# Kernel tuning notes

Hardware: AMD Instinct MI355X
Metric: run time of the kernel (lower is better)

Reference implementation:

```python
import jax, jax.numpy as jnp
import numpy as np

HEAD_NUM = 16

def setup_inputs() -> dict:
    key = jax.random.key(0)
    ks = jax.random.split(key, 5)
    B, N, D = 2, 2048, 1024
    x = jax.random.normal(ks[0], (B, N, D), dtype=jnp.float32)
    scale = 0.02
    W_q = jax.random.normal(ks[1], (D, D), dtype=jnp.float32) * scale
    W_k = jax.random.normal(ks[2], (D, D), dtype=jnp.float32) * scale
    W_v = jax.random.normal(ks[3], (D, D), dtype=jnp.float32) * scale
    W_o = jax.random.normal(ks[4], (D, D), dtype=jnp.float32) * scale
    return {"x": x, "W_q": W_q, "W_k": W_k, "W_v": W_v, "W_o": W_o}

def reference(x, W_q, W_k, W_v, W_o):
    B, N, D = x.shape
    H = HEAD_NUM
    hd = D // H  # head_dim
    inv_sqrt_hd = 1.0 / np.sqrt(hd).astype(np.float32)

    def split_head(t):
        # einops 'b n (d h) -> b h n d' : head index is the INNER factor
        return t.reshape(B, N, hd, H).transpose(0, 3, 1, 2)  # [B,H,N,hd]

    # nn.Linear(bias=False): y = x @ W.T
    Q = split_head(x @ W_q.T)
    K = split_head(x @ W_k.T)
    V = split_head(x @ W_v.T)

    scores = jnp.einsum('bhnd,bhmd->bhnm', Q, K) * inv_sqrt_hd  # [B,H,N,N]
    attn = jax.nn.softmax(scores, axis=-1)
    heads = jnp.einsum('bhnm,bhmd->bhnd', attn, V)  # [B,H,N,hd]

    # einops 'b h n d -> b n (h d)' : head index is the OUTER factor here
    concat = heads.transpose(0, 2, 1, 3).reshape(B, N, D)
    return concat @ W_o.T
```

## Files before the change

### kernel.cpp

```cpp
#include <hip/hip_runtime.h>
#include <hip/hip_bf16.h>

typedef __bf16 bf16_t;
typedef __attribute__((ext_vector_type(8))) __bf16 bf16x8;
typedef __attribute__((ext_vector_type(4))) __bf16 bf16x4;
typedef __attribute__((ext_vector_type(4))) float f32x4;
typedef __attribute__((ext_vector_type(16))) float f32x16;

#define MFMA16(A,B,C) __builtin_amdgcn_mfma_f32_16x16x32_bf16((A),(B),(C),0,0,0)
#define MFMA32(A,B,C) __builtin_amdgcn_mfma_f32_32x32x16_bf16((A),(B),(C),0,0,0)

#define BATCH 2
#define SEQ 2048
#define DMODEL 1024
#define NHEAD 16
#define HDIM 64
#define MROWS (BATCH * SEQ)

__device__ __forceinline__ void async16(const bf16_t* g, bf16_t* l) {
    __builtin_amdgcn_global_load_lds(
        (const __attribute__((address_space(1))) unsigned int*)g,
        (__attribute__((address_space(3))) unsigned int*)l, 16, 0, 0);
}

__device__ __forceinline__ bf16x8 ldsA32(const bf16_t* base, int row, int chunk) {
    return *(const bf16x8*)&base[row * 32 + ((chunk ^ ((row >> 1) & 3)) << 3)];
}

__device__ __forceinline__ unsigned pk(float a, float b) {
    union { unsigned u; bf16_t h[2]; } t;
    t.h[0] = (bf16_t)a;
    t.h[1] = (bf16_t)b;
    return t.u;
}

__global__ void split_kernel(const float* __restrict__ x, const float* __restrict__ Wq,
                             const float* __restrict__ Wk, const float* __restrict__ Wv,
                             const float* __restrict__ Wo, bf16_t* __restrict__ xh,
                             bf16_t* __restrict__ wh) {
    int blk = blockIdx.x;
    if (blk < 4096) {
        int i = blk * 256 + threadIdx.x;
        f32x4 v = ((const f32x4*)x)[i];
        bf16x4 h;
#pragma unroll
        for (int c = 0; c < 4; ++c) h[c] = (bf16_t)v[c];
        ((bf16x4*)xh)[i] = h;
        return;
    }
    int e = blk - 4096;
    int z = e >> 10;
    int i = (e & 1023) * 256 + threadIdx.x;
    const float* src = (z == 0) ? Wq : (z == 1) ? Wk : (z == 2) ? Wv : Wo;
    const float scale = (z == 0) ? 0.125f * 1.44269504088896f : 1.0f;
    int row = i >> 8, col4 = i & 255;
    int r_src;
    if (z < 3) {
        int h = row >> 6, d = row & 63;
        r_src = 16 * d + h;
    } else {
        r_src = row;
    }
    f32x4 v = ((const f32x4*)src)[r_src * 256 + col4];
    bf16x4 h4;
#pragma unroll
    for (int c = 0; c < 4; ++c) h4[c] = (bf16_t)(v[c] * scale);
    ((bf16x4*)(wh + (size_t)z * DMODEL * DMODEL))[i] = h4;
}

__global__ __launch_bounds__(256)
void gemm_qkv_kernel(const bf16_t* __restrict__ Ah, const bf16_t* __restrict__ Bh0,
                     bf16_t* __restrict__ Coh0, bf16_t* __restrict__ Vt,
                     int M, int Nn, int Kk) {
    __shared__ __align__(16) bf16_t smem[2][8192];

    const int id = blockIdx.x;
    const int xcd = id & 7;
    const int t = id >> 3;
    const int n0i = t & 7;
    const int u = t >> 3;
    const int z = u >> 2;
    const int m0g = u & 3;
    const int m0 = (m0g * 8 + xcd) * 128;
    const int n0 = n0i * 128;

    const bf16_t* Bh = Bh0 + (size_t)z * Nn * Kk;
    const int tid = threadIdx.x;
    const int wave = tid >> 6, lane = tid & 63, lq = lane >> 4, ln = lane & 15;
    const int wr = wave >> 1, wc = wave & 1;

    const bf16_t* g_ptr[4];
    int l_off[4];
#pragma unroll
    for (int q = 0; q < 4; ++q) {
        int e = wave * 4 + q;
        int a = e >> 3, uu = e & 7;
        int C = uu * 64 + lane;
        int r = C >> 2, p = C & 3;
        int c = p ^ ((r >> 1) & 3);
        g_ptr[q] = (a == 0 ? Ah + (size_t)(m0 + r) * Kk
                           : Bh + (size_t)(n0 + r) * Kk) + c * 8;
        l_off[q] = a * 4096 + uu * 512;
    }

    f32x4 acc[4][4] = {};

#pragma unroll
    for (int q = 0; q < 4; ++q)
        async16(g_ptr[q], &smem[0][l_off[q]]);

    const int NIT = Kk / 32;
    for (int j = 0; j < NIT; ++j) {
        __syncthreads();
        if (j + 1 < NIT) {
#pragma unroll
            for (int q = 0; q < 4; ++q)
                async16(g_ptr[q] + (j + 1) * 32, &smem[(j + 1) & 1][l_off[q]]);
        }
        const bf16_t* cur = smem[j & 1];

        bf16x8 ah[4], bh[4];
#pragma unroll
        for (int tt = 0; tt < 4; ++tt) {
            ah[tt] = ldsA32(cur, wr * 64 + tt * 16 + ln, lq);
            bh[tt] = ldsA32(cur + 4096, wc * 64 + tt * 16 + ln, lq);
        }
#pragma unroll
        for (int tm = 0; tm < 4; ++tm)
#pragma unroll
            for (int tn = 0; tn < 4; ++tn)
                acc[tm][tn] = MFMA16(ah[tm], bh[tn], acc[tm][tn]);
    }

    if (z != 2) {
#pragma unroll
        for (int tm = 0; tm < 4; ++tm)
#pragma unroll
            for (int tn = 0; tn < 4; ++tn)
#pragma unroll
                for (int p = 0; p < 4; ++p) {
                    int gm = m0 + wr * 64 + tm * 16 + lq * 4 + p;
                    int gn = n0 + wc * 64 + tn * 16 + ln;
                    Coh0[(size_t)z * M * Nn + (size_t)gm * Nn + gn] =
                        (bf16_t)acc[tm][tn][p];
                }
    } else {
#pragma unroll
        for (int tm = 0; tm < 4; ++tm)
#pragma unroll
            for (int tn = 0; tn < 4; ++tn) {
                int gn = n0 + wc * 64 + tn * 16 + ln;
                int hh = gn >> 6, dd = gn & 63;
                int gm0 = m0 + wr * 64 + tm * 16 + lq * 4;
                int bb = gm0 >> 11, nn = gm0 & 2047;
                bf16x4 v4;
#pragma unroll
                for (int p = 0; p < 4; ++p) v4[p] = (bf16_t)acc[tm][tn][p];
                *(bf16x4*)&Vt[(((size_t)(bb * NHEAD + hh)) * HDIM + dd) * SEQ + nn] = v4;
            }
    }
}

__global__ __launch_bounds__(256)
void gemm_out_kernel(const bf16_t* __restrict__ Ah, const bf16_t* __restrict__ Bh,
                     float* __restrict__ Cf, int M, int Nn, int Kk) {
    __shared__ __align__(16) bf16_t smem[2][6144];

    const int id = blockIdx.x;
    const int xcd = id & 7;
    const int t = id >> 3;
    const int n0i = t & 7;
    const int m0g = t >> 3;
    const int m0 = (m0g * 8 + xcd) * 64;
    const int n0 = n0i * 128;

    const int tid = threadIdx.x;
    const int wave = tid >> 6, lane = tid & 63, lq = lane >> 4, ln = lane & 15;
    const int wr = wave >> 1, wc = wave & 1;

    const bf16_t* g_ptr[3];
    int l_off[3];
#pragma unroll
    for (int q = 0; q < 3; ++q) {
        int e = wave * 3 + q;
        const bf16_t* arr;
        int u, rowbase, lb;
        if (e < 4) { arr = Ah; u = e;     rowbase = m0; lb = 0; }
        else       { arr = Bh; u = e - 4; rowbase = n0; lb = 2048; }
        int r = u * 16 + (lane >> 2), p = lane & 3;
        int c = p ^ ((r >> 1) & 3);
        g_ptr[q] = arr + (size_t)(rowbase + r) * Kk + c * 8;
        l_off[q] = lb + u * 512;
    }

    f32x4 acc[2][4] = {};

#pragma unroll
    for (int q = 0; q < 3; ++q)
        async16(g_ptr[q], &smem[0][l_off[q]]);

    const int NIT = Kk / 32;
    for (int j = 0; j < NIT; ++j) {
        __syncthreads();
        if (j + 1 < NIT) {
#pragma unroll
            for (int q = 0; q < 3; ++q)
                async16(g_ptr[q] + (j + 1) * 32, &smem[(j + 1) & 1][l_off[q]]);
        }
        const bf16_t* cur = smem[j & 1];

        bf16x8 ah[2], bh[4];
#pragma unroll
        for (int tt = 0; tt < 2; ++tt)
            ah[tt] = ldsA32(cur, wr * 32 + tt * 16 + ln, lq);
#pragma unroll
        for (int tt = 0; tt < 4; ++tt)
            bh[tt] = ldsA32(cur + 2048, wc * 64 + tt * 16 + ln, lq);
#pragma unroll
        for (int tm = 0; tm < 2; ++tm)
#pragma unroll
            for (int tn = 0; tn < 4; ++tn)
                acc[tm][tn] = MFMA16(ah[tm], bh[tn], acc[tm][tn]);
    }

#pragma unroll
    for (int tm = 0; tm < 2; ++tm)
#pragma unroll
        for (int tn = 0; tn < 4; ++tn)
#pragma unroll
            for (int p = 0; p < 4; ++p) {
                int gm = m0 + wr * 32 + tm * 16 + lq * 4 + p;
                int gn = n0 + wc * 64 + tn * 16 + ln;
                Cf[(size_t)gm * Nn + gn] = acc[tm][tn][p];
            }
}

__global__ __launch_bounds__(512, 4)
void attn_kernel(const bf16_t* __restrict__ Qh, const bf16_t* __restrict__ Kh,
                 const bf16_t* __restrict__ Vt, bf16_t* __restrict__ Ch) {
    __shared__ __align__(16) bf16_t smem[2][2][8192];

    const int id = blockIdx.x;
    const int bh = ((id >> 7) << 3) | (id & 7);
    const int qt = (id >> 3) & 15;
    const int b = bh >> 4, h = bh & 15;
    const int q0 = qt * 128;
    const int tid = threadIdx.x;
    const int g = tid >> 8;
    const int wv = (tid >> 6) & 3;
    const int lane = tid & 63;
    const int ln32 = lane & 31, hl = lane >> 5;

    bf16x8 qfh[4];
    {
        size_t qrow = ((size_t)(b * SEQ + q0 + wv * 32 + ln32)) * DMODEL +
                      h * HDIM + hl * 8;
#pragma unroll
        for (int c = 0; c < 4; ++c)
            qfh[c] = *(const bf16x8*)&Qh[qrow + c * 16];
    }

    const int xrow = ln32 * 64;
    int xc[4];
#pragma unroll
    for (int c = 0; c < 4; ++c)
        xc[c] = (((2 * c + hl) ^ (ln32 & 7)) << 3) + xrow;

    bf16_t* gsm = &smem[g][0][0];
    const bf16_t* g_cur[4];
    int l_off[4];
    size_t g_step[4];
#pragma unroll
    for (int q = 0; q < 4; ++q) {
        int e = wv * 4 + q;
        int a = e >> 3, u = e & 7;
        int r = u * 8 + (lane >> 3), p = lane & 7;
        int c = p ^ (r & 7);
        if (a == 0) {
            g_cur[q] = Kh + ((size_t)(b * SEQ + g * 1024 + r)) * DMODEL +
                       h * HDIM + c * 8;
            l_off[q] = u * 512;
            g_step[q] = (size_t)64 * DMODEL;
        } else {
            g_cur[q] = Vt + ((size_t)(bh * HDIM + r)) * SEQ + g * 1024 + c * 8;
            l_off[q] = 4096 + u * 512;
            g_step[q] = 64;
        }
    }

    f32x16 o[2];
#pragma unroll
    for (int dt = 0; dt < 2; ++dt)
#pragma unroll
        for (int r = 0; r < 16; ++r) o[dt][r] = 0.0f;
    float rs = 0.0f;

#pragma unroll
    for (int q = 0; q < 4; ++q) {
        async16(g_cur[q], gsm + l_off[q]);
        g_cur[q] += g_step[q];
    }

    for (int j = 0; j < 16; ++j) {
        __syncthreads();
        if (j < 15) {
#pragma unroll
            for (int q = 0; q < 4; ++q) {
                async16(g_cur[q], gsm + ((j + 1) & 1) * 8192 + l_off[q]);
                g_cur[q] += g_step[q];
            }
        }
        const bf16_t* Kc = gsm + (j & 1) * 8192;
        const bf16_t* Vc = Kc + 4096;

        bf16x8 pfrag[4];
#pragma unroll
        for (int kt = 0; kt < 2; ++kt) {
            f32x16 st;
#pragma unroll
            for (int r = 0; r < 16; ++r) st[r] = 0.0f;
#pragma unroll
            for (int c = 0; c < 4; ++c) {
                bf16x8 kh = *(const bf16x8*)&Kc[kt * 2048 + xc[c]];
                st = MFMA32(kh, qfh[c], st);
            }
            float pexp[16];
#pragma unroll
            for (int r = 0; r < 16; ++r) {
                pexp[r] = __builtin_amdgcn_exp2f(st[r]);
                rs += pexp[r];
            }
#pragma unroll
            for (int s1 = 0; s1 < 2; ++s1) {
                unsigned lo01 = pk(pexp[8 * s1 + 0], pexp[8 * s1 + 1]);
                unsigned lo23 = pk(pexp[8 * s1 + 2], pexp[8 * s1 + 3]);
                unsigned hi01 = pk(pexp[8 * s1 + 4], pexp[8 * s1 + 5]);
                unsigned hi23 = pk(pexp[8 * s1 + 6], pexp[8 * s1 + 7]);
                unsigned sa = hl ? lo01 : hi01;
                unsigned sb = hl ? lo23 : hi23;
                unsigned ra = (unsigned)__shfl_xor((int)sa, 32);
                unsigned rb = (unsigned)__shfl_xor((int)sb, 32);
                union { bf16x8 v; unsigned u[4]; } outv;
                outv.u[0] = hl ? ra : lo01;
                outv.u[1] = hl ? rb : lo23;
                outv.u[2] = hl ? hi01 : ra;
                outv.u[3] = hl ? hi23 : rb;
                pfrag[kt * 2 + s1] = outv.v;
            }
        }
#pragma unroll
        for (int s = 0; s < 4; ++s) {
            bf16x8 va0 = *(const bf16x8*)&Vc[xc[s]];
            bf16x8 va1 = *(const bf16x8*)&Vc[2048 + xc[s]];
            o[0] = MFMA32(va0, pfrag[s], o[0]);
            o[1] = MFMA32(va1, pfrag[s], o[1]);
        }
    }

    rs += __shfl_xor(rs, 32);

    __syncthreads();
    float* cbuf = (float*)smem;
    float* rbuf = cbuf + 8192;
    if (g == 1) {
#pragma unroll
        for (int dt = 0; dt < 2; ++dt)
#pragma unroll
            for (int r = 0; r < 16; ++r) {
                int d = dt * 32 + (r & 3) + 8 * (r >> 2) + 4 * hl;
                cbuf[d * 128 + wv * 32 + ln32] = o[dt][r];
            }
        if (hl == 0) rbuf[wv * 32 + ln32] = rs;
    }
    __syncthreads();
    float inv = 0.0f;
    if (g == 0) {
#pragma unroll
        for (int dt = 0; dt < 2; ++dt)
#pragma unroll
            for (int r = 0; r < 16; ++r) {
                int d = dt * 32 + (r & 3) + 8 * (r >> 2) + 4 * hl;
                o[dt][r] += cbuf[d * 128 + wv * 32 + ln32];
            }
        inv = 1.0f / (rs + rbuf[wv * 32 + ln32]);
    }
    __syncthreads();
    float* fbuf = (float*)smem;
    if (g == 0) {
#pragma unroll
        for (int dh = 0; dh < 2; ++dh)
#pragma unroll
            for (int r = 0; r < 16; ++r) {
                int d_loc = (r & 3) + 8 * (r >> 2) + 4 * hl;
                fbuf[dh * 4224 + wv * 1056 + ln32 * 33 + d_loc] = o[dh][r] * inv;
            }
    }
    __syncthreads();
    {
        int gw = tid >> 6;
        int dh = gw >> 2, w = gw & 3;
#pragma unroll
        for (int qq = 0; qq < 16; ++qq) {
            int qrow = hl * 16 + qq;
            float v = fbuf[dh * 4224 + w * 1056 + qrow * 33 + ln32];
            size_t gidx = ((size_t)(b * SEQ + q0 + w * 32 + qrow)) * DMODEL +
                          h * HDIM + dh * 32 + ln32;
            Ch[gidx] = (bf16_t)v;
        }
    }
}

extern "C" void kernel_launch(void* const* d_in, const int* in_sizes, int n_in,
                              void* d_out, int out_size, void* d_ws, size_t ws_size,
                              hipStream_t stream) {
    const float* x  = (const float*)d_in[0];
    const float* Wq = (const float*)d_in[1];
    const float* Wk = (const float*)d_in[2];
    const float* Wv = (const float*)d_in[3];
    const float* Wo = (const float*)d_in[4];
    float* out = (float*)d_out;

    char* ws = (char*)d_ws;
    size_t off = 0;
    auto alloc = [&](size_t bytes) -> bf16_t* {
        bf16_t* p = (bf16_t*)(ws + off);
        off += (bytes + 255) & ~(size_t)255;
        return p;
    };
    const size_t XE = (size_t)MROWS * DMODEL;
    const size_t WE = (size_t)DMODEL * DMODEL;

    bf16_t* xh  = alloc(XE * 2);
    bf16_t* wh  = alloc(4 * WE * 2);
    bf16_t* qnh = alloc(3 * XE * 2);
    bf16_t* vth = alloc(XE * 2);
    bf16_t* ch  = alloc(XE * 2);
    (void)ws_size; (void)in_sizes; (void)n_in; (void)out_size;

    split_kernel<<<8192, 256, 0, stream>>>(x, Wq, Wk, Wv, Wo, xh, wh);

    gemm_qkv_kernel<<<768, 256, 0, stream>>>(xh, wh, qnh, vth, MROWS, DMODEL, DMODEL);

    attn_kernel<<<512, 512, 0, stream>>>(qnh, qnh + XE, vth, ch);

    gemm_out_kernel<<<512, 256, 0, stream>>>(ch, wh + 3 * WE, out, MROWS, DMODEL, DMODEL);
}
```

Baseline: 179.4 us.

## Halve attention block threads, each wave computing two 32-row query tiles

The attention kernel now runs 256 threads (4 waves) per block instead of 512. Each wave handles two 32-query sub-tiles, so every K and V fragment read from LDS is reused across two MFMAs, and each wave issues twice as many async K/V loads. The aim is to cut LDS read traffic per MFMA and the per-wave overhead. In exchange, register pressure roughly doubles for accumulators and Q fragments, and there are fewer waves available to hide latency.

```diff
diff --git a/kernel.cpp b/kernel.cpp
--- a/kernel.cpp
+++ b/kernel.cpp
@@ -235,7 +235,7 @@
             }
 }
 
-__global__ __launch_bounds__(512, 4)
+__global__ __launch_bounds__(256, 2)
 void attn_kernel(const bf16_t* __restrict__ Qh, const bf16_t* __restrict__ Kh,
                  const bf16_t* __restrict__ Vt, bf16_t* __restrict__ Ch) {
     __shared__ __align__(16) bf16_t smem[2][2][8192];
@@ -246,18 +246,20 @@
     const int b = bh >> 4, h = bh & 15;
     const int q0 = qt * 128;
     const int tid = threadIdx.x;
-    const int g = tid >> 8;
-    const int wv = (tid >> 6) & 3;
+    const int wave = tid >> 6;
+    const int g = wave >> 1;
+    const int wg = wave & 1;
     const int lane = tid & 63;
     const int ln32 = lane & 31, hl = lane >> 5;
 
-    bf16x8 qfh[4];
-    {
-        size_t qrow = ((size_t)(b * SEQ + q0 + wv * 32 + ln32)) * DMODEL +
+    bf16x8 qfh[2][4];
+#pragma unroll
+    for (int s = 0; s < 2; ++s) {
+        size_t qrow = ((size_t)(b * SEQ + q0 + wg * 64 + s * 32 + ln32)) * DMODEL +
                       h * HDIM + hl * 8;
 #pragma unroll
         for (int c = 0; c < 4; ++c)
-            qfh[c] = *(const bf16x8*)&Qh[qrow + c * 16];
+            qfh[s][c] = *(const bf16x8*)&Qh[qrow + c * 16];
     }
 
     const int xrow = ln32 * 64;
@@ -267,12 +269,12 @@
         xc[c] = (((2 * c + hl) ^ (ln32 & 7)) << 3) + xrow;
 
     bf16_t* gsm = &smem[g][0][0];
-    const bf16_t* g_cur[4];
-    int l_off[4];
-    size_t g_step[4];
-#pragma unroll
-    for (int q = 0; q < 4; ++q) {
-        int e = wv * 4 + q;
+    const bf16_t* g_cur[8];
+    int l_off[8];
+    size_t g_step[8];
+#pragma unroll
+    for (int q = 0; q < 8; ++q) {
+        int e = wg * 8 + q;
         int a = e >> 3, u = e & 7;
         int r = u * 8 + (lane >> 3), p = lane & 7;
         int c = p ^ (r & 7);
@@ -288,15 +290,17 @@
         }
     }
 
-    f32x16 o[2];
-#pragma unroll
-    for (int dt = 0; dt < 2; ++dt)
-#pragma unroll
-        for (int r = 0; r < 16; ++r) o[dt][r] = 0.0f;
-    float rs = 0.0f;
-
-#pragma unroll
-    for (int q = 0; q < 4; ++q) {
+    f32x16 o[2][2];
+#pragma unroll
+    for (int s = 0; s < 2; ++s)
+#pragma unroll
+        for (int dt = 0; dt < 2; ++dt)
+#pragma unroll
+            for (int r = 0; r < 16; ++r) o[s][dt][r] = 0.0f;
+    float rs[2] = {0.0f, 0.0f};
+
+#pragma unroll
+    for (int q = 0; q < 8; ++q) {
         async16(g_cur[q], gsm + l_off[q]);
         g_cur[q] += g_step[q];
     }
@@ -305,7 +309,7 @@
         __syncthreads();
         if (j < 15) {
 #pragma unroll
-            for (int q = 0; q < 4; ++q) {
+            for (int q = 0; q < 8; ++q) {
                 async16(g_cur[q], gsm + ((j + 1) & 1) * 8192 + l_off[q]);
                 g_cur[q] += g_step[q];
             }
@@ -313,100 +317,121 @@
         const bf16_t* Kc = gsm + (j & 1) * 8192;
         const bf16_t* Vc = Kc + 4096;
 
-        bf16x8 pfrag[4];
+        bf16x8 pfrag[2][4];
 #pragma unroll
         for (int kt = 0; kt < 2; ++kt) {
-            f32x16 st;
-#pragma unroll
-            for (int r = 0; r < 16; ++r) st[r] = 0.0f;
+            f32x16 st0, st1;
+#pragma unroll
+            for (int r = 0; r < 16; ++r) { st0[r] = 0.0f; st1[r] = 0.0f; }
 #pragma unroll
             for (int c = 0; c < 4; ++c) {
                 bf16x8 kh = *(const bf16x8*)&Kc[kt * 2048 + xc[c]];
-                st = MFMA32(kh, qfh[c], st);
-            }
-            float pexp[16];
-#pragma unroll
-            for (int r = 0; r < 16; ++r) {
-                pexp[r] = __builtin_amdgcn_exp2f(st[r]);
-                rs += pexp[r];
-            }
-#pragma unroll
-            for (int s1 = 0; s1 < 2; ++s1) {
-                unsigned lo01 = pk(pexp[8 * s1 + 0], pexp[8 * s1 + 1]);
-                unsigned lo23 = pk(pexp[8 * s1 + 2], pexp[8 * s1 + 3]);
-                unsigned hi01 = pk(pexp[8 * s1 + 4], pexp[8 * s1 + 5]);
-                unsigned hi23 = pk(pexp[8 * s1 + 6], pexp[8 * s1 + 7]);
-                unsigned sa = hl ? lo01 : hi01;
-                unsigned sb = hl ? lo23 : hi23;
-                unsigned ra = (unsigned)__shfl_xor((int)sa, 32);
-                unsigned rb = (unsigned)__shfl_xor((int)sb, 32);
-                union { bf16x8 v; unsigned u[4]; } outv;
-                outv.u[0] = hl ? ra : lo01;
-                outv.u[1] = hl ? rb : lo23;
-                outv.u[2] = hl ? hi01 : ra;
-                outv.u[3] = hl ? hi23 : rb;
-                pfrag[kt * 2 + s1] = outv.v;
-            }
-        }
-#pragma unroll
-        for (int s = 0; s < 4; ++s) {
-            bf16x8 va0 = *(const bf16x8*)&Vc[xc[s]];
-            bf16x8 va1 = *(const bf16x8*)&Vc[2048 + xc[s]];
-            o[0] = MFMA32(va0, pfrag[s], o[0]);
-            o[1] = MFMA32(va1, pfrag[s], o[1]);
-        }
-    }
-
-    rs += __shfl_xor(rs, 32);
+                st0 = MFMA32(kh, qfh[0][c], st0);
+                st1 = MFMA32(kh, qfh[1][c], st1);
+            }
+#pragma unroll
+            for (int s = 0; s < 2; ++s) {
+                float pexp[16];
+#pragma unroll
+                for (int r = 0; r < 16; ++r) {
+                    pexp[r] = __builtin_amdgcn_exp2f(s == 0 ? st0[r] : st1[r]);
+                    rs[s] += pexp[r];
+                }
+#pragma unroll
+                for (int s1 = 0; s1 < 2; ++s1) {
+                    unsigned lo01 = pk(pexp[8 * s1 + 0], pexp[8 * s1 + 1]);
+                    unsigned lo23 = pk(pexp[8 * s1 + 2], pexp[8 * s1 + 3]);
+                    unsigned hi01 = pk(pexp[8 * s1 + 4], pexp[8 * s1 + 5]);
+                    unsigned hi23 = pk(pexp[8 * s1 + 6], pexp[8 * s1 + 7]);
+                    unsigned sa = hl ? lo01 : hi01;
+                    unsigned sb = hl ? lo23 : hi23;
+                    unsigned ra = (unsigned)__shfl_xor((int)sa, 32);
+                    unsigned rb = (unsigned)__shfl_xor((int)sb, 32);
+                    union { bf16x8 v; unsigned u[4]; } outv;
+                    outv.u[0] = hl ? ra : lo01;
+                    outv.u[1] = hl ? rb : lo23;
+                    outv.u[2] = hl ? hi01 : ra;
+                    outv.u[3] = hl ? hi23 : rb;
+                    pfrag[s][kt * 2 + s1] = outv.v;
+                }
+            }
+        }
+#pragma unroll
+        for (int sg = 0; sg < 4; ++sg) {
+            bf16x8 va0 = *(const bf16x8*)&Vc[xc[sg]];
+            bf16x8 va1 = *(const bf16x8*)&Vc[2048 + xc[sg]];
+            o[0][0] = MFMA32(va0, pfrag[0][sg], o[0][0]);
+            o[1][0] = MFMA32(va0, pfrag[1][sg], o[1][0]);
+            o[0][1] = MFMA32(va1, pfrag[0][sg], o[0][1]);
+            o[1][1] = MFMA32(va1, pfrag[1][sg], o[1][1]);
+        }
+    }
+
+    rs[0] += __shfl_xor(rs[0], 32);
+    rs[1] += __shfl_xor(rs[1], 32);
 
     __syncthreads();
     float* cbuf = (float*)smem;
     float* rbuf = cbuf + 8192;
     if (g == 1) {
 #pragma unroll
-        for (int dt = 0; dt < 2; ++dt)
-#pragma unroll
-            for (int r = 0; r < 16; ++r) {
-                int d = dt * 32 + (r & 3) + 8 * (r >> 2) + 4 * hl;
-                cbuf[d * 128 + wv * 32 + ln32] = o[dt][r];
-            }
-        if (hl == 0) rbuf[wv * 32 + ln32] = rs;
+        for (int s = 0; s < 2; ++s) {
+            int qcol = wg * 64 + s * 32 + ln32;
+#pragma unroll
+            for (int dt = 0; dt < 2; ++dt)
+#pragma unroll
+                for (int r = 0; r < 16; ++r) {
+                    int d = dt * 32 + (r & 3) + 8 * (r >> 2) + 4 * hl;
+                    cbuf[d * 128 + qcol] = o[s][dt][r];
+                }
+            if (hl == 0) rbuf[qcol] = rs[s];
+        }
     }
     __syncthreads();
-    float inv = 0.0f;
+    float inv[2] = {0.0f, 0.0f};
     if (g == 0) {
 #pragma unroll
-        for (int dt = 0; dt < 2; ++dt)
-#pragma unroll
-            for (int r = 0; r < 16; ++r) {
-                int d = dt * 32 + (r & 3) + 8 * (r >> 2) + 4 * hl;
-                o[dt][r] += cbuf[d * 128 + wv * 32 + ln32];
-            }
-        inv = 1.0f / (rs + rbuf[wv * 32 + ln32]);
+        for (int s = 0; s < 2; ++s) {
+            int qcol = wg * 64 + s * 32 + ln32;
+#pragma unroll
+            for (int dt = 0; dt < 2; ++dt)
+#pragma unroll
+                for (int r = 0; r < 16; ++r) {
+                    int d = dt * 32 + (r & 3) + 8 * (r >> 2) + 4 * hl;
+                    o[s][dt][r] += cbuf[d * 128 + qcol];
+                }
+            inv[s] = 1.0f / (rs[s] + rbuf[qcol]);
+        }
     }
     __syncthreads();
     float* fbuf = (float*)smem;
     if (g == 0) {
 #pragma unroll
-        for (int dh = 0; dh < 2; ++dh)
-#pragma unroll
-            for (int r = 0; r < 16; ++r) {
-                int d_loc = (r & 3) + 8 * (r >> 2) + 4 * hl;
-                fbuf[dh * 4224 + wv * 1056 + ln32 * 33 + d_loc] = o[dh][r] * inv;
-            }
+        for (int s = 0; s < 2; ++s) {
+            int v = wg * 2 + s;
+#pragma unroll
+            for (int dh = 0; dh < 2; ++dh)
+#pragma unroll
+                for (int r = 0; r < 16; ++r) {
+                    int d_loc = (r & 3) + 8 * (r >> 2) + 4 * hl;
+                    fbuf[dh * 4224 + v * 1056 + ln32 * 33 + d_loc] =
+                        o[s][dh][r] * inv[s];
+                }
+        }
     }
     __syncthreads();
     {
-        int gw = tid >> 6;
-        int dh = gw >> 2, w = gw & 3;
-#pragma unroll
-        for (int qq = 0; qq < 16; ++qq) {
-            int qrow = hl * 16 + qq;
-            float v = fbuf[dh * 4224 + w * 1056 + qrow * 33 + ln32];
-            size_t gidx = ((size_t)(b * SEQ + q0 + w * 32 + qrow)) * DMODEL +
-                          h * HDIM + dh * 32 + ln32;
-            Ch[gidx] = (bf16_t)v;
-        }
+        int v = wave;
+#pragma unroll
+        for (int dh = 0; dh < 2; ++dh)
+#pragma unroll
+            for (int qq = 0; qq < 16; ++qq) {
+                int qrow = hl * 16 + qq;
+                float val = fbuf[dh * 4224 + v * 1056 + qrow * 33 + ln32];
+                size_t gidx = ((size_t)(b * SEQ + q0 + v * 32 + qrow)) * DMODEL +
+                              h * HDIM + dh * 32 + ln32;
+                Ch[gidx] = (bf16_t)val;
+            }
     }
 }
 
@@ -441,7 +466,7 @@
 
     gemm_qkv_kernel<<<768, 256, 0, stream>>>(xh, wh, qnh, vth, MROWS, DMODEL, DMODEL);
 
-    attn_kernel<<<512, 512, 0, stream>>>(qnh, qnh + XE, vth, ch);
+    attn_kernel<<<512, 256, 0, stream>>>(qnh, qnh + XE, vth, ch);
 
     gemm_out_kernel<<<512, 256, 0, stream>>>(ch, wh + 3 * WE, out, MROWS, DMODEL, DMODEL);
 }
```

After: 180.6 us. No clear change (+0.7%).
